# Optimization experiments

Hardware: AMD Instinct MI355X
Metric: run time of the kernel (lower is better)

The kernel has to match this reference:

```python
import jax, jax.numpy as jnp
import numpy as np

EPS = 1e-7  # K.epsilon()

def setup_inputs() -> dict:
    key = jax.random.key(0)
    k1, k2, k3 = jax.random.split(key, 3)
    B, T, D = 32, 2048, 512
    x = jax.random.normal(k1, (B, T, D), dtype=jnp.float32)
    W = jax.random.normal(k2, (D, D), dtype=jnp.float32) * (1.0 / np.sqrt(D))
    b = jnp.zeros((D,), dtype=jnp.float32)
    u = jax.random.normal(k3, (D,), dtype=jnp.float32) * (1.0 / np.sqrt(D))
    return {"x": x, "W": W, "b": b, "u": u}

def reference(x, W, b, u):
    # uit = tanh(x @ W + b)  -> [B, T, D]
    uit = jnp.tanh(jnp.einsum('btd,de->bte', x, W) + b)
    # scores: sum over feature dim of uit * u -> [B, T]
    ait = jnp.einsum('btd,d->bt', uit, u)
    # exp + normalize over T (no mask); matches original exp/sum form
    a = jnp.exp(ait)
    a = a / (jnp.sum(a, axis=1, keepdims=True) + EPS)
    # weighted sum pooling over T -> [B, D]
    return jnp.einsum('btd,bt->bd', x, a)
```

## Files before the change

kernel.cpp:

```cpp
#include <hip/hip_runtime.h>
#include <math.h>

#define D_DIM 512

typedef short short8v __attribute__((ext_vector_type(8)));
typedef unsigned short ushort8v __attribute__((ext_vector_type(8)));
typedef unsigned short ushort4v __attribute__((ext_vector_type(4)));
typedef float f32x16 __attribute__((ext_vector_type(16)));

__device__ inline unsigned short f2bf(float f) {
    union { float f; unsigned int u; } a; a.f = f;
    unsigned int u = a.u;
    unsigned int r = (u + 0x7fffu + ((u >> 16) & 1u)) >> 16;
    return (unsigned short)r;
}

__device__ inline float fast_tanh(float y) {
    float e2 = __expf(2.f * y);
    return 1.f - __fdividef(2.f, e2 + 1.f);
}

__device__ inline unsigned ldsaddr(const void* p) {
    return (unsigned)(size_t)(__attribute__((address_space(3))) const void*)p;
}

__global__ __launch_bounds__(1024) void wt_kernel(const float* __restrict__ W,
                                                  unsigned short* __restrict__ Wb2,
                                                  float* __restrict__ zero_base,
                                                  int zero_count) {
    __shared__ __align__(16) unsigned short lbuf[16384];
    const int s = blockIdx.x;
    const int tid = threadIdx.x;
    if (s == 0) {
        for (int i = tid; i < zero_count; i += 1024) zero_base[i] = 0.f;
    }
    #pragma unroll
    for (int i = 0; i < 4; ++i) {
        int flat = tid + i * 1024;
        int kr = flat >> 7;
        int e4 = (flat & 127) * 4;
        float4 v = *(const float4*)(W + (size_t)(s * 32 + kr) * D_DIM + e4);
        int ks = kr >> 4, half = (kr >> 3) & 1, j = kr & 7;
        float vv[4] = {v.x, v.y, v.z, v.w};
        #pragma unroll
        for (int q = 0; q < 4; ++q) {
            int e = e4 + q, g = e >> 5, nl = e & 31;
            lbuf[ks * 8192 + ((g * 2 + half) * 32 + nl) * 8 + j] = f2bf(vv[q]);
        }
    }
    __syncthreads();
    #pragma unroll
    for (int i = 0; i < 2; ++i) {
        int c = tid + i * 1024;
        *(ushort8v*)(Wb2 + (size_t)s * 16384 + c * 8) = *(const ushort8v*)&lbuf[c * 8];
    }
}

__global__ __launch_bounds__(512, 2) void gemm_ait_fused(
    const float* __restrict__ x, const unsigned short* __restrict__ Wb2,
    const float* __restrict__ bias, const float* __restrict__ u,
    float* __restrict__ numer, float* __restrict__ denom, int T)
{
    __shared__ __align__(16) unsigned short xa[32768];
    __shared__ float rowpart[8][64];

    const int tid  = threadIdx.x;
    const int wave = tid >> 6;
    const int lane = tid & 63;
    const int half = lane >> 5;
    const int nl   = lane & 31;
    const int m0   = blockIdx.x * 64;

    f32x16 acc[2][2];
    #pragma unroll
    for (int mi = 0; mi < 2; ++mi)
        #pragma unroll
        for (int ni = 0; ni < 2; ++ni)
            #pragma unroll
            for (int r = 0; r < 16; ++r) acc[mi][ni][r] = 0.f;

    short8v a[2][2], b[2][2];

    const unsigned bvoff0 = (unsigned)(((wave * 4 + half) * 32 + nl) * 16);

    asm volatile("global_load_dwordx4 %0, %1, %2"
                 : "=v"(b[0][0]) : "v"(bvoff0), "s"(Wb2) : "memory");
    asm volatile("global_load_dwordx4 %0, %1, %2 offset:1024"
                 : "=v"(b[0][1]) : "v"(bvoff0), "s"(Wb2) : "memory");
    {
        unsigned v1 = bvoff0 + 16384u;
        asm volatile("global_load_dwordx4 %0, %1, %2"
                     : "=v"(b[1][0]) : "v"(v1), "s"(Wb2) : "memory");
        asm volatile("global_load_dwordx4 %0, %1, %2 offset:1024"
                     : "=v"(b[1][1]) : "v"(v1), "s"(Wb2) : "memory");
    }

    #pragma unroll
    for (int i = 0; i < 16; ++i) {
        int flat = tid + i * 512;
        int row = flat >> 7;
        int c4  = (flat & 127) * 4;
        float4 v = *(const float4*)(x + (size_t)(m0 + row) * D_DIM + c4);
        int ks = c4 >> 4, hf = (c4 >> 3) & 1, j0 = c4 & 7;
        int mi = row >> 5, r5 = row & 31;
        ushort4v pk;
        pk[0] = f2bf(v.x); pk[1] = f2bf(v.y); pk[2] = f2bf(v.z); pk[3] = f2bf(v.w);
        *(ushort4v*)&xa[(((ks * 2 + mi) * 2 + hf) * 32 + r5) * 8 + j0] = pk;
    }
    __syncthreads();

    const unsigned abase = ldsaddr(&xa[0]) + (unsigned)(half * 512 + nl * 16);
    asm volatile("ds_read_b128 %0, %1" : "=v"(a[0][0]) : "v"(abase) : "memory");
    asm volatile("ds_read_b128 %0, %1 offset:1024" : "=v"(a[0][1]) : "v"(abase) : "memory");

    #pragma unroll
    for (int s = 0; s < 32; ++s) {
        if (s < 31) { asm volatile("s_waitcnt vmcnt(2)" ::: "memory"); }
        else        { asm volatile("s_waitcnt vmcnt(0)" ::: "memory"); }
        __builtin_amdgcn_sched_barrier(0);
        if (s + 1 < 32) {
            unsigned ao = abase + (unsigned)((s + 1) * 2048);
            asm volatile("ds_read_b128 %0, %1" : "=v"(a[(s + 1) & 1][0]) : "v"(ao) : "memory");
            asm volatile("ds_read_b128 %0, %1 offset:1024" : "=v"(a[(s + 1) & 1][1]) : "v"(ao) : "memory");
            asm volatile("s_waitcnt lgkmcnt(2)" ::: "memory");
        } else {
            asm volatile("s_waitcnt lgkmcnt(0)" ::: "memory");
        }
        __builtin_amdgcn_sched_barrier(0);
        __builtin_amdgcn_s_setprio(1);
        acc[0][0] = __builtin_amdgcn_mfma_f32_32x32x16_bf16(a[s & 1][0], b[s & 1][0], acc[0][0], 0, 0, 0);
        acc[0][1] = __builtin_amdgcn_mfma_f32_32x32x16_bf16(a[s & 1][0], b[s & 1][1], acc[0][1], 0, 0, 0);
        acc[1][0] = __builtin_amdgcn_mfma_f32_32x32x16_bf16(a[s & 1][1], b[s & 1][0], acc[1][0], 0, 0, 0);
        acc[1][1] = __builtin_amdgcn_mfma_f32_32x32x16_bf16(a[s & 1][1], b[s & 1][1], acc[1][1], 0, 0, 0);
        __builtin_amdgcn_s_setprio(0);
        if (s + 2 < 32) {
            unsigned vo = bvoff0 + (unsigned)((s + 2) * 16384);
            asm volatile("global_load_dwordx4 %0, %1, %2"
                         : "=v"(b[s & 1][0]) : "v"(vo), "s"(Wb2) : "memory");
            asm volatile("global_load_dwordx4 %0, %1, %2 offset:1024"
                         : "=v"(b[s & 1][1]) : "v"(vo), "s"(Wb2) : "memory");
        }
    }

    float rowsum[2][16];
    #pragma unroll
    for (int mi = 0; mi < 2; ++mi)
        #pragma unroll
        for (int r = 0; r < 16; ++r) rowsum[mi][r] = 0.f;

    #pragma unroll
    for (int mi = 0; mi < 2; ++mi) {
        #pragma unroll
        for (int ni = 0; ni < 2; ++ni) {
            int col = wave * 64 + ni * 32 + nl;
            float be = bias[col], ue = u[col];
            #pragma unroll
            for (int r = 0; r < 16; ++r)
                rowsum[mi][r] += fast_tanh(acc[mi][ni][r] + be) * ue;
        }
    }
    #pragma unroll
    for (int mi = 0; mi < 2; ++mi)
        #pragma unroll
        for (int r = 0; r < 16; ++r) {
            float v = rowsum[mi][r];
            v += __shfl_xor(v, 1, 64);
            v += __shfl_xor(v, 2, 64);
            v += __shfl_xor(v, 4, 64);
            v += __shfl_xor(v, 8, 64);
            v += __shfl_xor(v, 16, 64);
            rowsum[mi][r] = v;
        }
    if (nl == 0) {
        #pragma unroll
        for (int mi = 0; mi < 2; ++mi)
            #pragma unroll
            for (int r = 0; r < 16; ++r) {
                int row = mi * 32 + (r & 3) + 8 * (r >> 2) + 4 * half;
                rowpart[wave][row] = rowsum[mi][r];
            }
    }
    __syncthreads();

    const int bidx = m0 / T;
    float* evals = (float*)&xa[0];
    if (tid < 64) {
        float s = 0.f;
        #pragma unroll
        for (int w = 0; w < 8; ++w) s += rowpart[w][tid];
        float e = __expf(s);
        evals[tid] = e;
        float t = e;
        t += __shfl_xor(t, 1, 64);
        t += __shfl_xor(t, 2, 64);
        t += __shfl_xor(t, 4, 64);
        t += __shfl_xor(t, 8, 64);
        t += __shfl_xor(t, 16, 64);
        t += __shfl_xor(t, 32, 64);
        if (tid == 0) atomicAdd(denom + bidx, t);
    }
    __syncthreads();

    const int dg = tid >> 7;
    const int d4 = (tid & 127) << 2;
    const float* xp = x + (size_t)m0 * D_DIM + d4;
    float4 pacc = {0.f, 0.f, 0.f, 0.f};
    #pragma unroll 4
    for (int r = dg; r < 64; r += 4) {
        float e = evals[r];
        float4 xv = *(const float4*)(xp + (size_t)r * D_DIM);
        pacc.x += e * xv.x; pacc.y += e * xv.y;
        pacc.z += e * xv.z; pacc.w += e * xv.w;
    }
    float4* ptmp = (float4*)&xa[256];
    if (dg > 0) ptmp[(dg - 1) * 128 + (tid & 127)] = pacc;
    __syncthreads();
    if (dg == 0) {
        float4 o0 = ptmp[tid], o1 = ptmp[128 + tid], o2 = ptmp[256 + tid];
        float* np = numer + (size_t)bidx * D_DIM + d4;
        atomicAdd(np + 0, pacc.x + o0.x + o1.x + o2.x);
        atomicAdd(np + 1, pacc.y + o0.y + o1.y + o2.y);
        atomicAdd(np + 2, pacc.z + o0.z + o1.z + o2.z);
        atomicAdd(np + 3, pacc.w + o0.w + o1.w + o2.w);
    }
}

__global__ __launch_bounds__(128) void out_div_kernel(
    const float* __restrict__ numer, const float* __restrict__ denom,
    float* __restrict__ out)
{
    const int b = blockIdx.x;
    const int tid = threadIdx.x;
    float inv = 1.0f / (denom[b] + 1e-7f);
    float4 v = *(const float4*)(numer + (size_t)b * D_DIM + tid * 4);
    v.x *= inv; v.y *= inv; v.z *= inv; v.w *= inv;
    *(float4*)(out + (size_t)b * D_DIM + tid * 4) = v;
}

__global__ __launch_bounds__(256) void gemm_ait_f32(
    const float* __restrict__ x, const float* __restrict__ W,
    const float* __restrict__ bias, const float* __restrict__ u,
    float* __restrict__ ait)
{
    __shared__ float xsf[64][68];
    __shared__ float wshf[64][132];
    const int tid = threadIdx.x;
    const int tx = tid & 15, ty = tid >> 4;
    const int m0 = blockIdx.x * 64;
    float rowsum[4] = {0.f, 0.f, 0.f, 0.f};
    for (int e0 = 0; e0 < D_DIM; e0 += 128) {
        float acc[4][8];
        #pragma unroll
        for (int i = 0; i < 4; ++i)
            #pragma unroll
            for (int j = 0; j < 8; ++j) acc[i][j] = 0.f;
        for (int kc = 0; kc < D_DIM; kc += 64) {
            #pragma unroll
            for (int i = 0; i < 4; ++i) {
                int idx = tid + i * 256;
                int r = idx >> 4, c = (idx & 15) * 4;
                *(float4*)&xsf[r][c] = *(const float4*)(x + (size_t)(m0 + r) * D_DIM + kc + c);
            }
            #pragma unroll
            for (int i = 0; i < 8; ++i) {
                int idx = tid + i * 256;
                int r = idx >> 5, c = (idx & 31) * 4;
                *(float4*)&wshf[r][c] = *(const float4*)(W + (size_t)(kc + r) * D_DIM + e0 + c);
            }
            __syncthreads();
            #pragma unroll 4
            for (int k = 0; k < 64; ++k) {
                float xv[4];
                #pragma unroll
                for (int i = 0; i < 4; ++i) xv[i] = xsf[ty * 4 + i][k];
                float4 w0 = *(const float4*)&wshf[k][tx * 8];
                float4 w1 = *(const float4*)&wshf[k][tx * 8 + 4];
                #pragma unroll
                for (int i = 0; i < 4; ++i) {
                    acc[i][0] += xv[i] * w0.x; acc[i][1] += xv[i] * w0.y;
                    acc[i][2] += xv[i] * w0.z; acc[i][3] += xv[i] * w0.w;
                    acc[i][4] += xv[i] * w1.x; acc[i][5] += xv[i] * w1.y;
                    acc[i][6] += xv[i] * w1.z; acc[i][7] += xv[i] * w1.w;
                }
            }
            __syncthreads();
        }
        #pragma unroll
        for (int j = 0; j < 8; ++j) {
            int e = e0 + tx * 8 + j;
            float be = bias[e], ue = u[e];
            #pragma unroll
            for (int i = 0; i < 4; ++i) rowsum[i] += tanhf(acc[i][j] + be) * ue;
        }
    }
    float* red = &xsf[0][0];
    #pragma unroll
    for (int i = 0; i < 4; ++i) red[(ty * 4 + i) * 16 + tx] = rowsum[i];
    __syncthreads();
    if (tid < 64) {
        float s = 0.f;
        #pragma unroll
        for (int j = 0; j < 16; ++j) s += red[tid * 16 + j];
        ait[m0 + tid] = s;
    }
}

__global__ __launch_bounds__(256) void softmax_kernel(float* __restrict__ ait, int T)
{
    const int b = blockIdx.x;
    float* p = ait + (size_t)b * T;
    const int tid = threadIdx.x;
    float ev[8];
    float local = 0.f;
    #pragma unroll
    for (int i = 0; i < 8; ++i) {
        ev[i] = expf(p[tid + i * 256]);
        local += ev[i];
    }
    #pragma unroll
    for (int off = 32; off > 0; off >>= 1)
        local += __shfl_down(local, off, 64);
    __shared__ float wsum[4];
    const int wv = tid >> 6, lane = tid & 63;
    if (lane == 0) wsum[wv] = local;
    __syncthreads();
    float total = wsum[0] + wsum[1] + wsum[2] + wsum[3];
    float inv = 1.0f / (total + 1e-7f);
    #pragma unroll
    for (int i = 0; i < 8; ++i) p[tid + i * 256] = ev[i] * inv;
}

__global__ __launch_bounds__(256) void pool_atomic_kernel(
    const float* __restrict__ x, const float* __restrict__ a,
    float* __restrict__ out, int T)
{
    const int chunks = T >> 8;
    const int b = blockIdx.x / chunks;
    const int c = blockIdx.x % chunks;
    const int tid = threadIdx.x;
    const int th = tid >> 7;
    const int d = (tid & 127) * 4;
    const float* xp = x + ((size_t)b * T + c * 256) * D_DIM + d;
    const float* ap = a + (size_t)b * T + c * 256;
    float4 acc = {0.f, 0.f, 0.f, 0.f};
    #pragma unroll 8
    for (int t = th; t < 256; t += 2) {
        float s = ap[t];
        float4 xv = *(const float4*)(xp + (size_t)t * D_DIM);
        acc.x += xv.x * s; acc.y += xv.y * s;
        acc.z += xv.z * s; acc.w += xv.w * s;
    }
    __shared__ float4 tmp[128];
    if (th == 1) tmp[tid & 127] = acc;
    __syncthreads();
    if (th == 0) {
        float4 o = tmp[tid];
        float* op = out + (size_t)b * D_DIM + tid * 4;
        atomicAdd(op + 0, acc.x + o.x);
        atomicAdd(op + 1, acc.y + o.y);
        atomicAdd(op + 2, acc.z + o.z);
        atomicAdd(op + 3, acc.w + o.w);
    }
}

extern "C" void kernel_launch(void* const* d_in, const int* in_sizes, int n_in,
                              void* d_out, int out_size, void* d_ws, size_t ws_size,
                              hipStream_t stream)
{
    const float* x    = (const float*)d_in[0];
    const float* W    = (const float*)d_in[1];
    const float* bias = (const float*)d_in[2];
    const float* u    = (const float*)d_in[3];
    float* out = (float*)d_out;

    const int Dd = in_sizes[2];
    const int M  = in_sizes[0] / Dd;
    const int B  = out_size / Dd;
    const int T  = M / B;
    const int chunks = T >> 8;

    const size_t wb_bytes  = (size_t)Dd * Dd * sizeof(unsigned short);
    const size_t ait_bytes = (size_t)M * sizeof(float);

    if (ws_size >= wb_bytes + ait_bytes) {
        unsigned short* Wb2 = (unsigned short*)d_ws;
        float* numer = (float*)((char*)d_ws + wb_bytes);
        float* denom = numer + (size_t)B * Dd;
        const int zero_count = B * Dd + B;

        wt_kernel<<<dim3(16), dim3(1024), 0, stream>>>(W, Wb2, numer, zero_count);
        gemm_ait_fused<<<dim3(M / 64), dim3(512), 0, stream>>>(x, Wb2, bias, u,
                                                               numer, denom, T);
        out_div_kernel<<<dim3(B), dim3(128), 0, stream>>>(numer, denom, out);
    } else {
        float* ait = (float*)d_ws;
        gemm_ait_f32<<<dim3(M / 64), dim3(256), 0, stream>>>(x, W, bias, u, ait);
        softmax_kernel<<<dim3(B), dim3(256), 0, stream>>>(ait, T);
        hipMemsetAsync(d_out, 0, (size_t)out_size * sizeof(float), stream);
        pool_atomic_kernel<<<dim3(B * chunks), dim3(256), 0, stream>>>(x, ait, out, T);
    }
}
```

Baseline: 243.8 us.

## Process two row tiles per block, prefetching next x tile during GEMM

Each block now handles 128 rows as two 64-row tiles, issuing global loads for the second tile's x inside the first tile's MFMA loop so the fetch overlaps compute. The LDS layout of the bf16 x tile is XOR-swizzled to cut bank conflicts on ds_read_b128. The fp32-to-bf16 packing now uses the hardware v_cvt_pk_bf16_f32 instruction. The cost is 64 extra VGPRs for the prefetched x, which may pressure occupancy at the 2-blocks-per-CU bound, and half as many blocks.

```diff
diff --git a/kernel.cpp b/kernel.cpp
--- a/kernel.cpp
+++ b/kernel.cpp
@@ -5,7 +5,6 @@
 
 typedef short short8v __attribute__((ext_vector_type(8)));
 typedef unsigned short ushort8v __attribute__((ext_vector_type(8)));
-typedef unsigned short ushort4v __attribute__((ext_vector_type(4)));
 typedef float f32x16 __attribute__((ext_vector_type(16)));
 
 __device__ inline unsigned short f2bf(float f) {
@@ -56,33 +55,28 @@
     }
 }
 
-__global__ __launch_bounds__(512, 2) void gemm_ait_fused(
-    const float* __restrict__ x, const unsigned short* __restrict__ Wb2,
-    const float* __restrict__ bias, const float* __restrict__ u,
-    float* __restrict__ numer, float* __restrict__ denom, int T)
-{
-    __shared__ __align__(16) unsigned short xa[32768];
-    __shared__ float rowpart[8][64];
-
-    const int tid  = threadIdx.x;
-    const int wave = tid >> 6;
-    const int lane = tid & 63;
-    const int half = lane >> 5;
-    const int nl   = lane & 31;
-    const int m0   = blockIdx.x * 64;
-
-    f32x16 acc[2][2];
-    #pragma unroll
-    for (int mi = 0; mi < 2; ++mi)
-        #pragma unroll
-        for (int ni = 0; ni < 2; ++ni)
-            #pragma unroll
-            for (int r = 0; r < 16; ++r) acc[mi][ni][r] = 0.f;
-
+__device__ __forceinline__ void pack_store(unsigned short* xa, int row, int c4, float4 v) {
+    int ks = c4 >> 4, hf = (c4 >> 3) & 1, j0 = c4 & 7;
+    int mi = row >> 5, r5 = row & 31;
+    unsigned byteoff = (unsigned)(((((ks * 2 + mi) * 2 + hf) * 32 + r5) * 8 + j0) * 2)
+                       ^ ((unsigned)((c4 >> 3) & 7) << 4);
+    unsigned lo, hi;
+    asm("v_cvt_pk_bf16_f32 %0, %1, %2" : "=v"(lo) : "v"(v.x), "v"(v.y));
+    asm("v_cvt_pk_bf16_f32 %0, %1, %2" : "=v"(hi) : "v"(v.z), "v"(v.w));
+    uint2 pk; pk.x = lo; pk.y = hi;
+    *(uint2*)((char*)xa + byteoff) = pk;
+}
+
+template<bool PREFX>
+__device__ __forceinline__ void run_ktile(
+    const unsigned short* __restrict__ Wb2,
+    unsigned bvoff0, unsigned abase2,
+    f32x16 (&acc)[2][2], float4 (&xnext)[16],
+    const float* x1base)
+{
     short8v a[2][2], b[2][2];
-
-    const unsigned bvoff0 = (unsigned)(((wave * 4 + half) * 32 + nl) * 16);
-
+    asm volatile("s_waitcnt vmcnt(0)" ::: "memory");
+    __builtin_amdgcn_sched_barrier(0);
     asm volatile("global_load_dwordx4 %0, %1, %2"
                  : "=v"(b[0][0]) : "v"(bvoff0), "s"(Wb2) : "memory");
     asm volatile("global_load_dwordx4 %0, %1, %2 offset:1024"
@@ -94,32 +88,25 @@
         asm volatile("global_load_dwordx4 %0, %1, %2 offset:1024"
                      : "=v"(b[1][1]) : "v"(v1), "s"(Wb2) : "memory");
     }
-
-    #pragma unroll
-    for (int i = 0; i < 16; ++i) {
-        int flat = tid + i * 512;
-        int row = flat >> 7;
-        int c4  = (flat & 127) * 4;
-        float4 v = *(const float4*)(x + (size_t)(m0 + row) * D_DIM + c4);
-        int ks = c4 >> 4, hf = (c4 >> 3) & 1, j0 = c4 & 7;
-        int mi = row >> 5, r5 = row & 31;
-        ushort4v pk;
-        pk[0] = f2bf(v.x); pk[1] = f2bf(v.y); pk[2] = f2bf(v.z); pk[3] = f2bf(v.w);
-        *(ushort4v*)&xa[(((ks * 2 + mi) * 2 + hf) * 32 + r5) * 8 + j0] = pk;
-    }
-    __syncthreads();
-
-    const unsigned abase = ldsaddr(&xa[0]) + (unsigned)(half * 512 + nl * 16);
-    asm volatile("ds_read_b128 %0, %1" : "=v"(a[0][0]) : "v"(abase) : "memory");
-    asm volatile("ds_read_b128 %0, %1 offset:1024" : "=v"(a[0][1]) : "v"(abase) : "memory");
+    asm volatile("ds_read_b128 %0, %1" : "=v"(a[0][0]) : "v"(abase2) : "memory");
+    asm volatile("ds_read_b128 %0, %1 offset:1024" : "=v"(a[0][1]) : "v"(abase2) : "memory");
 
     #pragma unroll
     for (int s = 0; s < 32; ++s) {
-        if (s < 31) { asm volatile("s_waitcnt vmcnt(2)" ::: "memory"); }
-        else        { asm volatile("s_waitcnt vmcnt(0)" ::: "memory"); }
+        if (PREFX) {
+            if (s == 0)       { asm volatile("s_waitcnt vmcnt(2)" ::: "memory"); }
+            else if (s == 1)  { asm volatile("s_waitcnt vmcnt(3)" ::: "memory"); }
+            else if (s <= 16) { asm volatile("s_waitcnt vmcnt(4)" ::: "memory"); }
+            else if (s == 17) { asm volatile("s_waitcnt vmcnt(3)" ::: "memory"); }
+            else if (s < 31)  { asm volatile("s_waitcnt vmcnt(2)" ::: "memory"); }
+            else              { asm volatile("s_waitcnt vmcnt(0)" ::: "memory"); }
+        } else {
+            if (s < 31)       { asm volatile("s_waitcnt vmcnt(2)" ::: "memory"); }
+            else              { asm volatile("s_waitcnt vmcnt(0)" ::: "memory"); }
+        }
         __builtin_amdgcn_sched_barrier(0);
         if (s + 1 < 32) {
-            unsigned ao = abase + (unsigned)((s + 1) * 2048);
+            unsigned ao = (abase2 + (unsigned)((s + 1) * 2048)) ^ (unsigned)((((s + 1) & 3)) << 5);
             asm volatile("ds_read_b128 %0, %1" : "=v"(a[(s + 1) & 1][0]) : "v"(ao) : "memory");
             asm volatile("ds_read_b128 %0, %1 offset:1024" : "=v"(a[(s + 1) & 1][1]) : "v"(ao) : "memory");
             asm volatile("s_waitcnt lgkmcnt(2)" ::: "memory");
@@ -140,8 +127,22 @@
             asm volatile("global_load_dwordx4 %0, %1, %2 offset:1024"
                          : "=v"(b[s & 1][1]) : "v"(vo), "s"(Wb2) : "memory");
         }
-    }
-
+        if (PREFX && s < 16) {
+            const float* xp = x1base + (size_t)s * 2048;
+            asm volatile("global_load_dwordx4 %0, %1, off"
+                         : "=v"(xnext[s]) : "v"(xp) : "memory");
+        }
+    }
+}
+
+__device__ __forceinline__ void epilogue_tile(
+    f32x16 (&acc)[2][2], int m0t, int T,
+    const float* __restrict__ bias, const float* __restrict__ u,
+    float* __restrict__ numer, float* __restrict__ denom,
+    const float* __restrict__ x,
+    unsigned short* xa, float (*rowpart)[64],
+    int tid, int wave, int half, int nl)
+{
     float rowsum[2][16];
     #pragma unroll
     for (int mi = 0; mi < 2; ++mi)
@@ -182,7 +183,7 @@
     }
     __syncthreads();
 
-    const int bidx = m0 / T;
+    const int bidx = m0t / T;
     float* evals = (float*)&xa[0];
     if (tid < 64) {
         float s = 0.f;
@@ -203,7 +204,7 @@
 
     const int dg = tid >> 7;
     const int d4 = (tid & 127) << 2;
-    const float* xp = x + (size_t)m0 * D_DIM + d4;
+    const float* xp = x + (size_t)m0t * D_DIM + d4;
     float4 pacc = {0.f, 0.f, 0.f, 0.f};
     #pragma unroll 4
     for (int r = dg; r < 64; r += 4) {
@@ -223,6 +224,73 @@
         atomicAdd(np + 2, pacc.z + o0.z + o1.z + o2.z);
         atomicAdd(np + 3, pacc.w + o0.w + o1.w + o2.w);
     }
+}
+
+__global__ __launch_bounds__(512, 2) void gemm_ait_fused(
+    const float* __restrict__ x, const unsigned short* __restrict__ Wb2,
+    const float* __restrict__ bias, const float* __restrict__ u,
+    float* __restrict__ numer, float* __restrict__ denom, int T)
+{
+    __shared__ __align__(128) unsigned short xa[32768];
+    __shared__ float rowpart[8][64];
+
+    const int tid  = threadIdx.x;
+    const int wave = tid >> 6;
+    const int lane = tid & 63;
+    const int half = lane >> 5;
+    const int nl   = lane & 31;
+    const int m0   = blockIdx.x * 128;
+
+    const unsigned bvoff0 = (unsigned)(((wave * 4 + half) * 32 + nl) * 16);
+    const unsigned abase2 = (ldsaddr(&xa[0]) + (unsigned)(half * 512 + nl * 16))
+                            ^ (unsigned)(half << 4);
+
+    float4 xnext[16];
+    f32x16 acc[2][2];
+
+    {
+        const float* x0 = x + (size_t)m0 * D_DIM;
+        #pragma unroll
+        for (int i = 0; i < 16; ++i) {
+            int flat = tid + i * 512;
+            int row = flat >> 7, c4 = (flat & 127) * 4;
+            float4 v = *(const float4*)(x0 + (size_t)row * D_DIM + c4);
+            pack_store(xa, row, c4, v);
+        }
+    }
+    __syncthreads();
+
+    #pragma unroll
+    for (int mi = 0; mi < 2; ++mi)
+        #pragma unroll
+        for (int ni = 0; ni < 2; ++ni)
+            #pragma unroll
+            for (int r = 0; r < 16; ++r) acc[mi][ni][r] = 0.f;
+
+    const float* x1base = x + (size_t)(m0 + 64 + (tid >> 7)) * D_DIM + (tid & 127) * 4;
+    run_ktile<true>(Wb2, bvoff0, abase2, acc, xnext, x1base);
+    epilogue_tile(acc, m0, T, bias, u, numer, denom, x, xa, rowpart,
+                  tid, wave, half, nl);
+    __syncthreads();
+
+    #pragma unroll
+    for (int i = 0; i < 16; ++i) {
+        int flat = tid + i * 512;
+        int row = flat >> 7, c4 = (flat & 127) * 4;
+        pack_store(xa, row, c4, xnext[i]);
+    }
+    __syncthreads();
+
+    #pragma unroll
+    for (int mi = 0; mi < 2; ++mi)
+        #pragma unroll
+        for (int ni = 0; ni < 2; ++ni)
+            #pragma unroll
+            for (int r = 0; r < 16; ++r) acc[mi][ni][r] = 0.f;
+
+    run_ktile<false>(Wb2, bvoff0, abase2, acc, xnext, x1base);
+    epilogue_tile(acc, m0 + 64, T, bias, u, numer, denom, x, xa, rowpart,
+                  tid, wave, half, nl);
 }
 
 __global__ __launch_bounds__(128) void out_div_kernel(
@@ -389,8 +457,8 @@
         const int zero_count = B * Dd + B;
 
         wt_kernel<<<dim3(16), dim3(1024), 0, stream>>>(W, Wb2, numer, zero_count);
-        gemm_ait_fused<<<dim3(M / 64), dim3(512), 0, stream>>>(x, Wb2, bias, u,
-                                                               numer, denom, T);
+        gemm_ait_fused<<<dim3(M / 128), dim3(512), 0, stream>>>(x, Wb2, bias, u,
+                                                                numer, denom, T);
         out_div_kernel<<<dim3(B), dim3(128), 0, stream>>>(numer, denom, out);
     } else {
         float* ait = (float*)d_ws;
```

Result: slower. 262.1 us (+7.5%).

## Split x tile staging and overlap second half with first MFMA steps

Applied to the files above, without the earlier changes.

The prologue now converts and stores only the first half of the K columns of the x tile into LDS before the MFMA loop starts. The second half is prefetched into registers with raw global loads and packed into LDS during loop iterations 4–7. A block barrier at step 15 makes those LDS writes visible before they are read. This hides part of the x load and bf16 conversion latency behind the GEMM, at the cost of 32 extra live VGPRs under a 2-blocks-per-CU launch bound, which may cause spills, plus one more barrier.

```diff
diff --git a/kernel.cpp b/kernel.cpp
--- a/kernel.cpp
+++ b/kernel.cpp
@@ -56,12 +56,20 @@
     }
 }
 
+__device__ __forceinline__ void pack_store(unsigned short* xa, int row, int c4, float4 v) {
+    int ks = c4 >> 4, hf = (c4 >> 3) & 1, j0 = c4 & 7;
+    int mi = row >> 5, r5 = row & 31;
+    ushort4v pk;
+    pk[0] = f2bf(v.x); pk[1] = f2bf(v.y); pk[2] = f2bf(v.z); pk[3] = f2bf(v.w);
+    *(ushort4v*)&xa[(((ks * 2 + mi) * 2 + hf) * 32 + r5) * 8 + j0] = pk;
+}
+
 __global__ __launch_bounds__(512, 2) void gemm_ait_fused(
     const float* __restrict__ x, const unsigned short* __restrict__ Wb2,
     const float* __restrict__ bias, const float* __restrict__ u,
     float* __restrict__ numer, float* __restrict__ denom, int T)
 {
-    __shared__ __align__(16) unsigned short xa[32768];
+    __shared__ __align__(128) unsigned short xa[32768];
     __shared__ float rowpart[8][64];
 
     const int tid  = threadIdx.x;
@@ -80,8 +88,20 @@
             for (int r = 0; r < 16; ++r) acc[mi][ni][r] = 0.f;
 
     short8v a[2][2], b[2][2];
+    float4 xh[8];
 
     const unsigned bvoff0 = (unsigned)(((wave * 4 + half) * 32 + nl) * 16);
+    const unsigned abase = ldsaddr(&xa[0]) + (unsigned)(half * 512 + nl * 16);
+
+    const float* x0 = x + (size_t)m0 * D_DIM;
+
+    #pragma unroll
+    for (int i = 0; i < 8; ++i) {
+        int chunk = tid + i * 512;
+        const float* p = x0 + (size_t)(chunk >> 6) * D_DIM + ((chunk & 63) * 4 + 256);
+        asm volatile("global_load_dwordx4 %0, %1, off"
+                     : "=v"(xh[i]) : "v"(p) : "memory");
+    }
 
     asm volatile("global_load_dwordx4 %0, %1, %2"
                  : "=v"(b[0][0]) : "v"(bvoff0), "s"(Wb2) : "memory");
@@ -96,25 +116,25 @@
     }
 
     #pragma unroll
-    for (int i = 0; i < 16; ++i) {
-        int flat = tid + i * 512;
-        int row = flat >> 7;
-        int c4  = (flat & 127) * 4;
-        float4 v = *(const float4*)(x + (size_t)(m0 + row) * D_DIM + c4);
-        int ks = c4 >> 4, hf = (c4 >> 3) & 1, j0 = c4 & 7;
-        int mi = row >> 5, r5 = row & 31;
-        ushort4v pk;
-        pk[0] = f2bf(v.x); pk[1] = f2bf(v.y); pk[2] = f2bf(v.z); pk[3] = f2bf(v.w);
-        *(ushort4v*)&xa[(((ks * 2 + mi) * 2 + hf) * 32 + r5) * 8 + j0] = pk;
-    }
-    __syncthreads();
-
-    const unsigned abase = ldsaddr(&xa[0]) + (unsigned)(half * 512 + nl * 16);
+    for (int i = 0; i < 8; ++i) {
+        int chunk = tid + i * 512;
+        int row = chunk >> 6;
+        int c4  = (chunk & 63) * 4;
+        float4 v = *(const float4*)(x0 + (size_t)row * D_DIM + c4);
+        pack_store(xa, row, c4, v);
+    }
+    __syncthreads();
+
     asm volatile("ds_read_b128 %0, %1" : "=v"(a[0][0]) : "v"(abase) : "memory");
     asm volatile("ds_read_b128 %0, %1 offset:1024" : "=v"(a[0][1]) : "v"(abase) : "memory");
 
     #pragma unroll
     for (int s = 0; s < 32; ++s) {
+        if (s == 15) {
+            asm volatile("s_waitcnt lgkmcnt(0)" ::: "memory");
+            __builtin_amdgcn_sched_barrier(0);
+            __builtin_amdgcn_s_barrier();
+        }
         if (s < 31) { asm volatile("s_waitcnt vmcnt(2)" ::: "memory"); }
         else        { asm volatile("s_waitcnt vmcnt(0)" ::: "memory"); }
         __builtin_amdgcn_sched_barrier(0);
@@ -139,6 +159,14 @@
                          : "=v"(b[s & 1][0]) : "v"(vo), "s"(Wb2) : "memory");
             asm volatile("global_load_dwordx4 %0, %1, %2 offset:1024"
                          : "=v"(b[s & 1][1]) : "v"(vo), "s"(Wb2) : "memory");
+        }
+        if (s >= 4 && s < 8) {
+            #pragma unroll
+            for (int k = 0; k < 2; ++k) {
+                int i = (s - 4) * 2 + k;
+                int chunk = tid + i * 512;
+                pack_store(xa, chunk >> 6, (chunk & 63) * 4 + 256, xh[i]);
+            }
         }
     }
 
```

After: 255.0 us. 1.05x slower.
